# Performance work log

Hardware: AMD Instinct MI355X
Metric: run time of the kernel (lower is better)

The kernel has to match this reference:

```python
import jax, jax.numpy as jnp
import numpy as np

N_HEAD = 4
N_FEAT = 256
D_K = N_FEAT // N_HEAD
MAX_SEQ_LEN = 500
LN_EPS = 1e-6


def setup_inputs() -> dict:
    key = jax.random.key(0)
    ks = jax.random.split(key, 12)
    B, L, F = 64, 500, N_FEAT
    s = lambda fan_in: 1.0 / np.sqrt(fan_in)
    return {
        "q": jax.random.normal(ks[0], (B, L, F), jnp.float32),
        "k": jax.random.normal(ks[1], (B, L, F), jnp.float32),
        "v": jax.random.normal(ks[2], (B, L, F), jnp.float32),
        # weights stored as [in, out] (torch Linear transposed)
        "w_qs": jax.random.normal(ks[3], (F, F), jnp.float32) * s(F),
        "w_vs": jax.random.normal(ks[4], (F, F), jnp.float32) * s(F),
        "w1": jax.random.normal(ks[5], (D_K, D_K), jnp.float32) * s(D_K),
        "b1": jax.random.normal(ks[6], (D_K,), jnp.float32) * s(D_K),
        "w2": jax.random.normal(ks[7], (D_K, MAX_SEQ_LEN), jnp.float32) * s(D_K),
        "b2": jax.random.normal(ks[8], (MAX_SEQ_LEN,), jnp.float32) * s(D_K),
        "fc_w": jax.random.normal(ks[9], (F, F), jnp.float32) * s(F),
        "ln_g": jnp.ones((F,), jnp.float32),
        "ln_b": jnp.zeros((F,), jnp.float32),
    }


def reference(q, k, v, w_qs, w_vs, w1, b1, w2, b2, fc_w, ln_g, ln_b):
    B, L, F = q.shape
    H, dk = N_HEAD, D_K
    residual = q
    # head projections -> [B, H, L, dk]
    qh = (q @ w_qs).reshape(B, L, H, dk).transpose(0, 2, 1, 3)
    vh = (v @ w_vs).reshape(B, L, H, dk).transpose(0, 2, 1, 3)
    # dense synthesizer: relu(q W1 + b1) W2 + b2, slice to len_q
    weight = jax.nn.relu(qh @ w1 + b1)
    attn = (weight @ w2 + b2)[..., :L]            # [B, H, L, L]
    attn = jax.nn.softmax(attn, axis=-1)
    out = attn @ vh                                # [B, H, L, dk]
    out = out.transpose(0, 2, 1, 3).reshape(B, L, F)
    out = out @ fc_w + residual
    # LayerNorm(eps=1e-6)
    mu = jnp.mean(out, axis=-1, keepdims=True)
    var = jnp.var(out, axis=-1, keepdims=True)
    out = (out - mu) * jax.lax.rsqrt(var + LN_EPS) * ln_g + ln_b
    return out
```

## Files before the change

### kernel.cpp

```cpp
#include <hip/hip_runtime.h>
#include <math.h>

#define B_   64
#define L_   500
#define F_   256
#define H_   4
#define DK   64
#define LOG2E 1.44269504088896340736f

typedef unsigned short u16;
typedef unsigned int   u32;
typedef __attribute__((ext_vector_type(8))) short short8;
typedef __attribute__((ext_vector_type(4))) float f32x4;

static __device__ __forceinline__ u16 f2bf(float f) {
    u32 u = __float_as_uint(f);
    u32 r = (u + 0x7FFFu + ((u >> 16) & 1u)) >> 16;
    return (u16)r;
}
static __device__ __forceinline__ u32 pk_bf16_up(float x, float y) {
    u32 xb = __float_as_uint(x) + 0x8000u;
    u32 yb = __float_as_uint(y) + 0x8000u;
    return (xb >> 16) | (yb & 0xFFFF0000u);
}
static __device__ __forceinline__ float exp2_fast(float x) {
#if __has_builtin(__builtin_amdgcn_exp2f)
    return __builtin_amdgcn_exp2f(x);
#else
    return exp2f(x);
#endif
}

typedef __attribute__((address_space(3))) u32 lds32;
typedef const __attribute__((address_space(1))) u32 gbl32;
static __device__ __forceinline__ void gload_lds16(const u16* g, u16* l) {
    __builtin_amdgcn_global_load_lds((gbl32*)g, (lds32*)l, 16, 0, 0);
}

__global__ __launch_bounds__(256) void prep_kernel(
    const float* __restrict__ wq, const float* __restrict__ wv,
    const float* __restrict__ fcw, const float* __restrict__ w1,
    const float* __restrict__ w2, const float* __restrict__ b2,
    u16* __restrict__ wqf, u16* __restrict__ wvf, u16* __restrict__ fcwT,
    u16* __restrict__ w1T, u16* __restrict__ w2sw,
    u16* __restrict__ qh_bf, u16* __restrict__ vhT, float* __restrict__ b2p)
{
    int t = blockIdx.x * 256 + threadIdx.x;
    int stride = gridDim.x * 256;
    for (int i = t; i < 256 * 256; i += stride) {
        int n = i >> 8, k = i & 255;
        fcwT[i] = f2bf(fcw[k * 256 + n]);
    }
    for (int i = t; i < 65536; i += stride) {
        int j  = i & 7;
        int ln = (i >> 3) & 63;
        int tn = (i >> 9) & 15;
        int ks = (i >> 13) & 1;
        int kc = i >> 14;
        int k  = kc * 64 + ks * 32 + (ln >> 4) * 8 + j;
        int n  = tn * 16 + (ln & 15);
        wqf[i] = f2bf(wq[k * 256 + n]);
        wvf[i] = f2bf(wv[k * 256 + n]);
    }
    for (int i = t; i < 64 * 64; i += stride) {
        int n = i >> 6, k = i & 63;
        w1T[i] = f2bf(w1[k * 64 + n]);
    }
    for (int i = t; i < 512 * 64; i += stride) {
        int cc  = i >> 12;
        int row = (i >> 6) & 63;
        int kc  = i & 63;
        int n   = cc * 64 + row;
        int kl  = kc ^ ((row & 7) << 3);
        w2sw[i] = f2bf((n < 500 ? w2[kl * 500 + n] : 0.f) * LOG2E);
    }
    for (int i = t; i < 512; i += stride)
        b2p[i] = (i < 500) ? b2[i] * LOG2E : -1e30f;
    for (int i = t; i < 3072; i += stride)
        qh_bf[8192000 + i] = 0;
    for (int i = t; i < 196608; i += stride) {
        int bh = i / 768;
        int r  = i - bh * 768;
        int d  = r / 12;
        int kk = 52 + (r - d * 12);
        vhT[((size_t)((bh * 8 + 7) * 64 + d)) * 64 + (kk ^ ((d & 7) << 3))] = 0;
    }
}

__global__ __launch_bounds__(512) void proj_kernel(
    const float* __restrict__ q, const float* __restrict__ v,
    const u16* __restrict__ wqf, const u16* __restrict__ wvf,
    u16* __restrict__ qh_bf, u16* __restrict__ vhT)
{
    const int which = blockIdx.y;
    const float* __restrict__ x = which ? v : q;
    const u16*   __restrict__ wf = which ? wvf : wqf;

    __shared__ __align__(16) u16 Xs[2][64][72];

    const int tid  = threadIdx.x;
    const int wvid = tid >> 6, ln = tid & 63;
    const int n16  = ln & 15, quad = ln >> 4;
    const int wr   = wvid >> 2, wc = wvid & 3;
    const int row0 = blockIdx.x * 64;

    f32x4 acc[2][4];
    #pragma unroll
    for (int mt = 0; mt < 2; mt++)
        #pragma unroll
        for (int nt = 0; nt < 4; nt++) acc[mt][nt] = (f32x4){0.f, 0.f, 0.f, 0.f};

    #pragma unroll
    for (int j = 0; j < 2; j++) {
        int idx = tid + 512 * j;
        int m = idx >> 4, k4 = idx & 15;
        float4 a = *(const float4*)&x[(size_t)(row0 + m) * 256 + k4 * 4];
        *(uint2*)&Xs[0][m][k4 * 4] =
            make_uint2(pk_bf16_up(a.x, a.y), pk_bf16_up(a.z, a.w));
    }
    __syncthreads();

    #pragma unroll
    for (int kc = 0; kc < 4; kc++) {
        const int cur = kc & 1;
        if (kc < 3) {
            #pragma unroll
            for (int j = 0; j < 2; j++) {
                int idx = tid + 512 * j;
                int m = idx >> 4, k4 = idx & 15;
                float4 a = *(const float4*)&x[(size_t)(row0 + m) * 256 +
                                              (kc + 1) * 64 + k4 * 4];
                *(uint2*)&Xs[cur ^ 1][m][k4 * 4] =
                    make_uint2(pk_bf16_up(a.x, a.y), pk_bf16_up(a.z, a.w));
            }
        }
        #pragma unroll
        for (int ks = 0; ks < 2; ks++) {
            short8 af[2];
            #pragma unroll
            for (int mt = 0; mt < 2; mt++)
                af[mt] = *(const short8*)&Xs[cur][wr * 32 + mt * 16 + n16]
                                            [ks * 32 + quad * 8];
            #pragma unroll
            for (int nt = 0; nt < 4; nt++) {
                const u16* fp = wf + ((((kc * 2 + ks) * 16) + (wc * 4 + nt)) * 64
                                      + ln) * 8;
                short8 bfr = *(const short8*)fp;
                #pragma unroll
                for (int mt = 0; mt < 2; mt++)
                    acc[mt][nt] = __builtin_amdgcn_mfma_f32_16x16x32_bf16(
                        af[mt], bfr, acc[mt][nt], 0, 0, 0);
            }
        }
        __syncthreads();
    }

    if (which == 0) {
        #pragma unroll
        for (int mt = 0; mt < 2; mt++) {
            int m0 = row0 + wr * 32 + mt * 16 + quad * 4;
            int b  = m0 / 500;
            int l0 = m0 - 500 * b;
            #pragma unroll
            for (int nt = 0; nt < 4; nt++) {
                int d = nt * 16 + n16;
                u16* dst = qh_bf + ((size_t)((b * 4 + wc) * 500 + l0)) * 64 + d;
                #pragma unroll
                for (int i = 0; i < 4; i++)
                    dst[(size_t)i * 64] = f2bf(acc[mt][nt][i]);
            }
        }
    } else {
        #pragma unroll
        for (int mt = 0; mt < 2; mt++) {
            int m0 = row0 + wr * 32 + mt * 16 + quad * 4;
            int b  = m0 / 500;
            int l0 = m0 - 500 * b;
            int vc = l0 >> 6, kk2 = l0 & 63;
            #pragma unroll
            for (int nt = 0; nt < 4; nt++) {
                int d = nt * 16 + n16;
                __align__(8) u16 t4[4];
                #pragma unroll
                for (int i = 0; i < 4; i++) t4[i] = f2bf(acc[mt][nt][i]);
                size_t base = ((size_t)(((b * 4 + wc) * 8 + vc) * 64 + d)) * 64;
                *(uint2*)&vhT[base + (kk2 ^ ((d & 7) << 3))] = *(const uint2*)t4;
            }
        }
    }
}

__global__ __launch_bounds__(512, 1) void attn_kernel(
    const u16* __restrict__ qh, const u16* __restrict__ vhT,
    const u16* __restrict__ w1T, const float* __restrict__ b1,
    const u16* __restrict__ w2sw, const float* __restrict__ b2p,
    u16* __restrict__ ctx)
{
    __shared__ __align__(16) u16 w2all[32768];
    __shared__ __align__(16) u16 v_s[2][4096];
    __shared__ __align__(16) float b2s[512];
    __shared__ __align__(16) u16 scr[8][4][16][72];

    const int tid  = threadIdx.x;
    const int wv   = tid >> 6;
    const int ln   = tid & 63;
    const int n16  = ln & 15;
    const int quad = ln >> 4;
    const int bh   = blockIdx.x;
    const int r0   = wv * 64;

    const u16* vg = vhT + (size_t)bh * 32768;

    {
        int base = wv * 4096;
        #pragma unroll
        for (int j = 0; j < 8; j++)
            gload_lds16(w2sw + base + j * 512 + ln * 8, &w2all[base + j * 512]);
        gload_lds16(vg + wv * 512 + ln * 8, &v_s[0][wv * 512]);
        if (wv < 2)
            gload_lds16((const u16*)b2p + wv * 512 + ln * 8, (u16*)&b2s[wv * 256]);
    }

    const int b = bh >> 2, h = bh & 3;

    {
        short8 a0[4], a1[4];
        #pragma unroll
        for (int rg = 0; rg < 4; rg++) {
            const u16* qbase =
                qh + ((size_t)(bh * 500 + r0 + rg * 16 + n16)) * 64;
            a0[rg] = *(const short8*)(qbase + quad * 8);
            a1[rg] = *(const short8*)(qbase + 32 + quad * 8);
        }
        #pragma unroll
        for (int nt = 0; nt < 4; nt++) {
            const u16* wb = w1T + (nt * 16 + n16) * 64;
            short8 wA0 = *(const short8*)(wb + quad * 8);
            short8 wA1 = *(const short8*)(wb + 32 + quad * 8);
            float4 bv = *(const float4*)&b1[nt * 16 + quad * 4];
            #pragma unroll
            for (int rg = 0; rg < 4; rg++) {
                f32x4 c = {bv.x, bv.y, bv.z, bv.w};
                c = __builtin_amdgcn_mfma_f32_16x16x32_bf16(wA0, a0[rg], c, 0, 0, 0);
                c = __builtin_amdgcn_mfma_f32_16x16x32_bf16(wA1, a1[rg], c, 0, 0, 0);
                u32 p01 = pk_bf16_up(fmaxf(c[0], 0.f), fmaxf(c[1], 0.f));
                u32 p23 = pk_bf16_up(fmaxf(c[2], 0.f), fmaxf(c[3], 0.f));
                *(uint2*)&scr[wv][rg][n16][nt * 16 + quad * 4] =
                    make_uint2(p01, p23);
            }
        }
    }
    short8 sa0[4], sa1[4];
    #pragma unroll
    for (int rg = 0; rg < 4; rg++) {
        sa0[rg] = *(const short8*)&scr[wv][rg][n16][quad * 8];
        sa1[rg] = *(const short8*)&scr[wv][rg][n16][32 + quad * 8];
    }

    f32x4 oacc[4][4];
    #pragma unroll
    for (int rg = 0; rg < 4; rg++)
        #pragma unroll
        for (int nt = 0; nt < 4; nt++)
            oacc[rg][nt] = (f32x4){0.f, 0.f, 0.f, 0.f};
    float sm[4] = {0.f, 0.f, 0.f, 0.f};

    __syncthreads();

    #pragma unroll 2
    for (int cc = 0; cc < 8; cc++) {
        if (cc < 7)
            gload_lds16(vg + (cc + 1) * 4096 + wv * 512 + ln * 8,
                        &v_s[(cc + 1) & 1][wv * 512]);
        const u16* vbuf = &v_s[cc & 1][0];

        #pragma unroll
        for (int t = 0; t < 4; t++) {
            int r  = t * 16 + n16;
            int sw = (r & 7) << 3;
            const u16* wb = &w2all[cc * 4096 + r * 64];
            short8 wA0 = *(const short8*)&wb[(quad * 8) ^ sw];
            short8 wA1 = *(const short8*)&wb[(32 + quad * 8) ^ sw];
            float4 bv = *(const float4*)&b2s[cc * 64 + t * 16 + quad * 4];
            #pragma unroll
            for (int rg = 0; rg < 4; rg++) {
                f32x4 c = {bv.x, bv.y, bv.z, bv.w};
                c = __builtin_amdgcn_mfma_f32_16x16x32_bf16(wA0, sa0[rg], c, 0, 0, 0);
                c = __builtin_amdgcn_mfma_f32_16x16x32_bf16(wA1, sa1[rg], c, 0, 0, 0);
                float e0 = exp2_fast(c[0]);
                float e1 = exp2_fast(c[1]);
                float e2 = exp2_fast(c[2]);
                float e3 = exp2_fast(c[3]);
                sm[rg] += (e0 + e1) + (e2 + e3);
                *(uint2*)&scr[wv][rg][n16][t * 16 + quad * 4] =
                    make_uint2(pk_bf16_up(e0, e1), pk_bf16_up(e2, e3));
            }
        }
        #pragma unroll
        for (int ks = 0; ks < 2; ks++) {
            short8 pa[4];
            #pragma unroll
            for (int rg = 0; rg < 4; rg++)
                pa[rg] = *(const short8*)&scr[wv][rg][n16][ks * 32 + quad * 8];
            #pragma unroll
            for (int nt = 0; nt < 4; nt++) {
                int d   = nt * 16 + n16;
                int swd = (d & 7) << 3;
                short8 vb = *(const short8*)&vbuf[d * 64 +
                                                  ((ks * 32 + quad * 8) ^ swd)];
                #pragma unroll
                for (int rg = 0; rg < 4; rg++)
                    oacc[rg][nt] = __builtin_amdgcn_mfma_f32_16x16x32_bf16(
                        pa[rg], vb, oacc[rg][nt], 0, 0, 0);
            }
        }
        __syncthreads();
    }

    #pragma unroll
    for (int rg = 0; rg < 4; rg++) {
        float smt = sm[rg];
        smt += __shfl_xor(smt, 16);
        smt += __shfl_xor(smt, 32);
        #pragma unroll
        for (int i = 0; i < 4; i++) {
            int lrow = r0 + rg * 16 + quad * 4 + i;
            float si = __shfl(smt, quad * 4 + i);
            if (lrow < 500) {
                float s = 1.f / si;
                u16* dst = &ctx[((size_t)(b * 500 + lrow)) * 256 + h * 64];
                #pragma unroll
                for (int nt = 0; nt < 4; nt++)
                    dst[nt * 16 + n16] = f2bf(oacc[rg][nt][i] * s);
            }
        }
    }
}

__global__ __launch_bounds__(512) void final_kernel(
    const u16* __restrict__ ctx, const u16* __restrict__ fcwT,
    const float* __restrict__ qres, const float* __restrict__ g,
    const float* __restrict__ bta, float* __restrict__ out)
{
    __shared__ u16 Xs[64][72];
    __shared__ u16 Ws[256][72];
    __shared__ float red[4][2][64];
    __shared__ float murs[2][64];

    const int tid  = threadIdx.x;
    const int wvid = tid >> 6, ln = tid & 63;
    const int n16  = ln & 15, quad = ln >> 4;
    const int wr   = wvid >> 2, wc = wvid & 3;
    const int row0 = blockIdx.x * 64;

    f32x4 acc[2][4];
    #pragma unroll
    for (int mt = 0; mt < 2; mt++)
        #pragma unroll
        for (int nt = 0; nt < 4; nt++) acc[mt][nt] = (f32x4){0.f, 0.f, 0.f, 0.f};

    for (int kc = 0; kc < 256; kc += 64) {
        {
            int idx = tid;
            int m = idx >> 3, k8 = idx & 7;
            *(uint4*)&Xs[m][k8 * 8] =
                *(const uint4*)&ctx[(size_t)(row0 + m) * 256 + kc + k8 * 8];
        }
        #pragma unroll
        for (int j = 0; j < 4; j++) {
            int idx = tid + 512 * j;
            int n = idx >> 3, k8 = idx & 7;
            *(uint4*)&Ws[n][k8 * 8] = *(const uint4*)&fcwT[n * 256 + kc + k8 * 8];
        }
        __syncthreads();
        #pragma unroll
        for (int ks = 0; ks < 2; ks++) {
            short8 af[2], bfr[4];
            #pragma unroll
            for (int mt = 0; mt < 2; mt++)
                af[mt] = *(const short8*)&Xs[wr * 32 + mt * 16 + n16][ks * 32 + quad * 8];
            #pragma unroll
            for (int nt = 0; nt < 4; nt++)
                bfr[nt] = *(const short8*)&Ws[wc * 64 + nt * 16 + n16][ks * 32 + quad * 8];
            #pragma unroll
            for (int mt = 0; mt < 2; mt++)
                #pragma unroll
                for (int nt = 0; nt < 4; nt++)
                    acc[mt][nt] = __builtin_amdgcn_mfma_f32_16x16x32_bf16(
                        af[mt], bfr[nt], acc[mt][nt], 0, 0, 0);
        }
        __syncthreads();
    }

    #pragma unroll
    for (int mt = 0; mt < 2; mt++) {
        int m0 = row0 + wr * 32 + mt * 16 + quad * 4;
        #pragma unroll
        for (int i = 0; i < 4; i++) {
            const float* rp = &qres[(size_t)(m0 + i) * 256 + wc * 64 + n16];
            #pragma unroll
            for (int nt = 0; nt < 4; nt++)
                acc[mt][nt][i] += rp[nt * 16];
        }
    }
    #pragma unroll
    for (int mt = 0; mt < 2; mt++) {
        #pragma unroll
        for (int i = 0; i < 4; i++) {
            float s1 = 0.f, s2 = 0.f;
            #pragma unroll
            for (int nt = 0; nt < 4; nt++) {
                float vv = acc[mt][nt][i];
                s1 += vv; s2 += vv * vv;
            }
            #pragma unroll
            for (int off = 1; off < 16; off <<= 1) {
                s1 += __shfl_xor(s1, off);
                s2 += __shfl_xor(s2, off);
            }
            if (n16 == 0) {
                int r = wr * 32 + mt * 16 + quad * 4 + i;
                red[wc][0][r] = s1;
                red[wc][1][r] = s2;
            }
        }
    }
    __syncthreads();
    if (tid < 64) {
        float S1 = red[0][0][tid] + red[1][0][tid] + red[2][0][tid] + red[3][0][tid];
        float S2 = red[0][1][tid] + red[1][1][tid] + red[2][1][tid] + red[3][1][tid];
        float mu  = S1 * 0.00390625f;
        float var = S2 * 0.00390625f - mu * mu;
        murs[0][tid] = mu;
        murs[1][tid] = rsqrtf(var + 1e-6f);
    }
    __syncthreads();

    float gv[4], bv[4];
    #pragma unroll
    for (int nt = 0; nt < 4; nt++) {
        int col = wc * 64 + nt * 16 + n16;
        gv[nt] = g[col];
        bv[nt] = bta[col];
    }
    #pragma unroll
    for (int mt = 0; mt < 2; mt++) {
        int rb = wr * 32 + mt * 16 + quad * 4;
        #pragma unroll
        for (int i = 0; i < 4; i++) {
            float mu = murs[0][rb + i];
            float rs = murs[1][rb + i];
            float* op = &out[(size_t)(row0 + rb + i) * 256 + wc * 64 + n16];
            #pragma unroll
            for (int nt = 0; nt < 4; nt++)
                op[nt * 16] = (acc[mt][nt][i] - mu) * rs * gv[nt] + bv[nt];
        }
    }
}

extern "C" void kernel_launch(void* const* d_in, const int* in_sizes, int n_in,
                              void* d_out, int out_size, void* d_ws, size_t ws_size,
                              hipStream_t stream)
{
    const float* q   = (const float*)d_in[0];
    const float* v   = (const float*)d_in[2];
    const float* wqs = (const float*)d_in[3];
    const float* wvs = (const float*)d_in[4];
    const float* w1  = (const float*)d_in[5];
    const float* b1  = (const float*)d_in[6];
    const float* w2  = (const float*)d_in[7];
    const float* b2  = (const float*)d_in[8];
    const float* fcw = (const float*)d_in[9];
    const float* lng = (const float*)d_in[10];
    const float* lnb = (const float*)d_in[11];
    float* out = (float*)d_out;

    u16* qh_bf = (u16*)d_ws;
    u16* vhT   = qh_bf + 8200192;
    u16* w1T   = vhT + 8388608;
    u16* w2sw  = w1T + 4096;
    u16* wqf   = w2sw + 32768;
    u16* wvf   = wqf + 65536;
    u16* fcwT  = wvf + 65536;
    u16* ctx   = fcwT + 65536;
    float* b2p = (float*)(qh_bf + 8195072);

    prep_kernel <<<dim3(64),     256, 0, stream>>>(wqs, wvs, fcw, w1, w2, b2,
                                                   wqf, wvf, fcwT, w1T, w2sw,
                                                   qh_bf, vhT, b2p);
    proj_kernel <<<dim3(500, 2), 512, 0, stream>>>(q, v, wqf, wvf, qh_bf, vhT);
    attn_kernel <<<dim3(256),    512, 0, stream>>>(qh_bf, vhT, w1T, b1, w2sw, b2p, ctx);
    final_kernel<<<dim3(500),    512, 0, stream>>>(ctx, fcwT, q, lng, lnb, out);
}
```

Baseline: 85.24 us.

## Restructure projection kernel to per-wave 16-row tiles with register-held activations

The projection GEMM now has each wavefront own 16 input rows across all 256 output columns. It loads the full row slice directly from global memory into registers as bf16 MFMA fragments, with no shared-memory staging and no block barriers. The q and v projections are merged into one 1D grid of 256-thread blocks with an occupancy hint. This drops LDS traffic and __syncthreads, but every wave now re-reads the whole weight matrix from global/L2, and the uncoalesced per-lane row loads may cost bandwidth.

```diff
diff --git a/kernel.cpp b/kernel.cpp
--- a/kernel.cpp
+++ b/kernel.cpp
@@ -87,105 +87,78 @@
     }
 }
 
-__global__ __launch_bounds__(512) void proj_kernel(
+__global__ __launch_bounds__(256, 4) void proj_kernel(
     const float* __restrict__ q, const float* __restrict__ v,
     const u16* __restrict__ wqf, const u16* __restrict__ wvf,
     u16* __restrict__ qh_bf, u16* __restrict__ vhT)
 {
-    const int which = blockIdx.y;
-    const float* __restrict__ x = which ? v : q;
+    const int tid  = threadIdx.x;
+    const int wv   = tid >> 6, ln = tid & 63;
+    const int n16  = ln & 15, quad = ln >> 4;
+    const int t    = blockIdx.x * 4 + wv;
+    const int which = (t >= 2000) ? 1 : 0;
+    const int r0   = (t - 2000 * which) * 16;
+    const float* __restrict__ x  = which ? v : q;
     const u16*   __restrict__ wf = which ? wvf : wqf;
 
-    __shared__ __align__(16) u16 Xs[2][64][72];
-
-    const int tid  = threadIdx.x;
-    const int wvid = tid >> 6, ln = tid & 63;
-    const int n16  = ln & 15, quad = ln >> 4;
-    const int wr   = wvid >> 2, wc = wvid & 3;
-    const int row0 = blockIdx.x * 64;
-
-    f32x4 acc[2][4];
-    #pragma unroll
-    for (int mt = 0; mt < 2; mt++)
-        #pragma unroll
-        for (int nt = 0; nt < 4; nt++) acc[mt][nt] = (f32x4){0.f, 0.f, 0.f, 0.f};
-
-    #pragma unroll
-    for (int j = 0; j < 2; j++) {
-        int idx = tid + 512 * j;
-        int m = idx >> 4, k4 = idx & 15;
-        float4 a = *(const float4*)&x[(size_t)(row0 + m) * 256 + k4 * 4];
-        *(uint2*)&Xs[0][m][k4 * 4] =
-            make_uint2(pk_bf16_up(a.x, a.y), pk_bf16_up(a.z, a.w));
-    }
-    __syncthreads();
-
-    #pragma unroll
-    for (int kc = 0; kc < 4; kc++) {
-        const int cur = kc & 1;
-        if (kc < 3) {
-            #pragma unroll
-            for (int j = 0; j < 2; j++) {
-                int idx = tid + 512 * j;
-                int m = idx >> 4, k4 = idx & 15;
-                float4 a = *(const float4*)&x[(size_t)(row0 + m) * 256 +
-                                              (kc + 1) * 64 + k4 * 4];
-                *(uint2*)&Xs[cur ^ 1][m][k4 * 4] =
-                    make_uint2(pk_bf16_up(a.x, a.y), pk_bf16_up(a.z, a.w));
-            }
-        }
-        #pragma unroll
-        for (int ks = 0; ks < 2; ks++) {
-            short8 af[2];
-            #pragma unroll
-            for (int mt = 0; mt < 2; mt++)
-                af[mt] = *(const short8*)&Xs[cur][wr * 32 + mt * 16 + n16]
-                                            [ks * 32 + quad * 8];
-            #pragma unroll
-            for (int nt = 0; nt < 4; nt++) {
-                const u16* fp = wf + ((((kc * 2 + ks) * 16) + (wc * 4 + nt)) * 64
-                                      + ln) * 8;
-                short8 bfr = *(const short8*)fp;
-                #pragma unroll
-                for (int mt = 0; mt < 2; mt++)
-                    acc[mt][nt] = __builtin_amdgcn_mfma_f32_16x16x32_bf16(
-                        af[mt], bfr, acc[mt][nt], 0, 0, 0);
-            }
-        }
-        __syncthreads();
+    short8 af[8];
+    {
+        const float* xrow = x + (size_t)(r0 + n16) * 256 + quad * 8;
+        #pragma unroll
+        for (int kq = 0; kq < 8; kq++) {
+            float4 xa = *(const float4*)(xrow + kq * 32);
+            float4 xb = *(const float4*)(xrow + kq * 32 + 4);
+            union { short8 s; u32 u[4]; } tc;
+            tc.u[0] = pk_bf16_up(xa.x, xa.y);
+            tc.u[1] = pk_bf16_up(xa.z, xa.w);
+            tc.u[2] = pk_bf16_up(xb.x, xb.y);
+            tc.u[3] = pk_bf16_up(xb.z, xb.w);
+            af[kq] = tc.s;
+        }
     }
 
     if (which == 0) {
-        #pragma unroll
-        for (int mt = 0; mt < 2; mt++) {
-            int m0 = row0 + wr * 32 + mt * 16 + quad * 4;
-            int b  = m0 / 500;
-            int l0 = m0 - 500 * b;
-            #pragma unroll
-            for (int nt = 0; nt < 4; nt++) {
-                int d = nt * 16 + n16;
-                u16* dst = qh_bf + ((size_t)((b * 4 + wc) * 500 + l0)) * 64 + d;
-                #pragma unroll
-                for (int i = 0; i < 4; i++)
-                    dst[(size_t)i * 64] = f2bf(acc[mt][nt][i]);
-            }
+        size_t base_i[4];
+        #pragma unroll
+        for (int i = 0; i < 4; i++) {
+            int m  = r0 + quad * 4 + i;
+            int b  = m / 500;
+            int l0 = m - 500 * b;
+            base_i[i] = (size_t)(b * 2000 + l0) * 64 + n16;
+        }
+        #pragma unroll
+        for (int tn = 0; tn < 16; tn++) {
+            f32x4 c = {0.f, 0.f, 0.f, 0.f};
+            #pragma unroll
+            for (int kq = 0; kq < 8; kq++) {
+                short8 bfr = *(const short8*)&wf[(((kq * 16 + tn) * 64) + ln) * 8];
+                c = __builtin_amdgcn_mfma_f32_16x16x32_bf16(af[kq], bfr, c, 0, 0, 0);
+            }
+            size_t hoff = (size_t)(tn >> 2) * 32000 + (tn & 3) * 16;
+            #pragma unroll
+            for (int i = 0; i < 4; i++)
+                qh_bf[base_i[i] + hoff] = f2bf(c[i]);
         }
     } else {
-        #pragma unroll
-        for (int mt = 0; mt < 2; mt++) {
-            int m0 = row0 + wr * 32 + mt * 16 + quad * 4;
-            int b  = m0 / 500;
-            int l0 = m0 - 500 * b;
-            int vc = l0 >> 6, kk2 = l0 & 63;
-            #pragma unroll
-            for (int nt = 0; nt < 4; nt++) {
-                int d = nt * 16 + n16;
-                __align__(8) u16 t4[4];
-                #pragma unroll
-                for (int i = 0; i < 4; i++) t4[i] = f2bf(acc[mt][nt][i]);
-                size_t base = ((size_t)(((b * 4 + wc) * 8 + vc) * 64 + d)) * 64;
-                *(uint2*)&vhT[base + (kk2 ^ ((d & 7) << 3))] = *(const uint2*)t4;
-            }
+        int m0  = r0 + quad * 4;
+        int b   = m0 / 500;
+        int l00 = m0 - 500 * b;
+        int vc  = l00 >> 6, kk = l00 & 63;
+        size_t base = (size_t)b * 131072 + (size_t)vc * 4096;
+        #pragma unroll
+        for (int tn = 0; tn < 16; tn++) {
+            f32x4 c = {0.f, 0.f, 0.f, 0.f};
+            #pragma unroll
+            for (int kq = 0; kq < 8; kq++) {
+                short8 bfr = *(const short8*)&wf[(((kq * 16 + tn) * 64) + ln) * 8];
+                c = __builtin_amdgcn_mfma_f32_16x16x32_bf16(af[kq], bfr, c, 0, 0, 0);
+            }
+            int d = (tn & 3) * 16 + n16;
+            __align__(8) u16 t4[4];
+            #pragma unroll
+            for (int i = 0; i < 4; i++) t4[i] = f2bf(c[i]);
+            *(uint2*)&vhT[base + (size_t)(tn >> 2) * 32768 + d * 64 +
+                          (kk ^ ((d & 7) << 3))] = *(const uint2*)t4;
         }
     }
 }
@@ -488,7 +461,7 @@
     prep_kernel <<<dim3(64),     256, 0, stream>>>(wqs, wvs, fcw, w1, w2, b2,
                                                    wqf, wvf, fcwT, w1T, w2sw,
                                                    qh_bf, vhT, b2p);
-    proj_kernel <<<dim3(500, 2), 512, 0, stream>>>(q, v, wqf, wvf, qh_bf, vhT);
+    proj_kernel <<<dim3(1000),   256, 0, stream>>>(q, v, wqf, wvf, qh_bf, vhT);
     attn_kernel <<<dim3(256),    512, 0, stream>>>(qh_bf, vhT, w1T, b1, w2sw, b2p, ctx);
     final_kernel<<<dim3(500),    512, 0, stream>>>(ctx, fcwT, q, lng, lnb, out);
 }
```

New measurement: 99.94 us. +17.2%, slower.
